# Optimization experiments

Measured on AMD Instinct MI355X. Metric: run time of the kernel, lower is better.

The kernel has to match this reference:

```python
import jax, jax.numpy as jnp
import numpy as np

B, S, H, E, C, V = 512, 256, 768, 6, 10, 3


def setup_inputs() -> dict:
    key = jax.random.key(0)
    ks = jax.random.split(key, 16)

    def w(k, shape):
        fan_in = shape[-1]
        return jax.random.normal(k, shape, dtype=jnp.float32) / np.sqrt(fan_in)

    return {
        'x': jax.random.randint(ks[0], (B, S), 0, V, dtype=jnp.int64),
        'emb': w(ks[1], (V, E)),
        'W_fx': w(ks[2], (H, E)), 'W_fh': w(ks[3], (H, H)), 'b_f': w(ks[4], (H, 1)),
        'W_ix': w(ks[5], (H, E)), 'W_ih': w(ks[6], (H, H)), 'b_i': w(ks[7], (H, 1)),
        'W_ox': w(ks[8], (H, E)), 'W_oh': w(ks[9], (H, H)), 'b_o': w(ks[10], (H, 1)),
        'W_cx': w(ks[11], (H, E)), 'b_c': w(ks[12], (H, 1)),
        'W_ph': w(ks[13], (C, H)), 'b_p': w(ks[14], (C, 1)),
        'c_init': jax.random.normal(ks[15], (H, B), dtype=jnp.float32) / np.sqrt(B),
    }


def reference(x, emb, W_fx, W_fh, b_f, W_ix, W_ih, b_i, W_ox, W_oh, b_o,
              W_cx, b_c, W_ph, b_p, c_init):
    # Embed tokens: [B, S] -> [B, S, E] -> time-major [S, E, B]
    xe = jnp.transpose(emb[x], (1, 2, 0))
    xs = xe[: S - 1]  # loop runs seq_length - 1 steps

    def step(carry, x_t):
        c_prev, _ = carry  # c_prev: [H, B], x_t: [E, B]
        f_t = jax.nn.sigmoid(W_fx @ x_t + W_fh @ c_prev + b_f)
        i_t = jax.nn.sigmoid(W_ix @ x_t + W_ih @ c_prev + b_i)
        o_t = jax.nn.sigmoid(W_ox @ x_t + W_oh @ c_prev + b_o)
        c_t = jax.nn.sigmoid(W_cx @ x_t + b_c) * i_t + c_prev * f_t
        h_t = jnp.tanh(c_t) * o_t
        return (c_t, h_t), None

    h0 = jnp.zeros((H, B), dtype=c_init.dtype)
    (c_fin, h_fin), _ = jax.lax.scan(step, (c_init, h0), xs)
    p_t = W_ph @ h_fin + b_p  # [C, B]
    return jax.nn.log_softmax(p_t.T, axis=-1)  # [B, C]
```

## Files before the change

### kernel.cpp

```cpp
#include <hip/hip_runtime.h>


typedef _Float16 f16x8 __attribute__((ext_vector_type(8)));
typedef _Float16 f16x4 __attribute__((ext_vector_type(4)));
typedef float    f32x4 __attribute__((ext_vector_type(4)));

#define Hdim  768
#define Bdim  512
#define Sdim  256
#define NSTEP 255
#define Edim  6
#define NCls  10
#define NGRP  16
#define NRB   12
#define GC    32
#define HB    64
#define NKK   24
#define NK2   12
#define CSTR  776
#define XSTR  260
#define ZSTR  33
#define PLANE (Bdim * Hdim)
#define SCL      4096.0f
#define SCL_INV  2.44140625e-4f

#define WP_FRAGS   (2 * NRB * 4 * NKK * 64)
#define WS_CBUF    0u
#define WS_HFIN    (2u * 2u * PLANE * 2u)
#define WS_BAR     (WS_HFIN + Bdim * Hdim * 4u)
#define WS_WPK     (WS_BAR + 4096u)
#define WS_BAR_BYTES (NGRP * 16u * 4u)

__device__ __forceinline__ float sigf(float z) { return 1.0f / (1.0f + __expf(-z)); }

__device__ __forceinline__ f32x4 mf(f16x8 a, f16x8 b, f32x4 c) {
    return __builtin_amdgcn_mfma_f32_16x16x32_f16(a, b, c, 0, 0, 0);
}

__device__ __forceinline__ void keepalive(f16x8& x) {
    asm volatile("" : "+v"(x));
}

__global__ void __launch_bounds__(256)
prep_w(const float* __restrict__ Wfh, const float* __restrict__ Wih,
       _Float16* __restrict__ wpk)
{
    const int fid  = blockIdx.x * 256 + threadIdx.x;
    const int lane = fid & 63;
    const int t1   = fid >> 6;
    const int kk   = t1 % NKK;
    const int gi   = t1 / NKK;
    const int sub  = gi & 3;
    const int t3   = gi >> 2;
    const int rb   = t3 % NRB;
    const int gate = t3 / NRB;
    const int q = lane >> 4, r = lane & 15;
    const int row = rb * 64 + sub * 16 + r;
    const int col = kk * 32 + q * 8;
    const float* src = (gate ? Wih : Wfh) + (size_t)row * Hdim + col;
    f16x8 hi, lo;
    #pragma unroll
    for (int j = 0; j < 8; ++j) {
        const float v = src[j];
        const _Float16 h = (_Float16)v;
        hi[j] = h;
        lo[j] = (_Float16)((v - (float)h) * SCL);
    }
    *(f16x8*)&wpk[(size_t)fid * 8] = hi;
    *(f16x8*)&wpk[((size_t)WP_FRAGS + fid) * 8] = lo;
}

__global__ void __launch_bounds__(512, 1)
lstm_persist(const int* __restrict__ xk, const float* __restrict__ emb,
             const float* __restrict__ Wfx, const float* __restrict__ bfv,
             const float* __restrict__ Wix, const float* __restrict__ biv,
             const float* __restrict__ Wox, const float* __restrict__ Woh,
             const float* __restrict__ bov,
             const float* __restrict__ Wcx, const float* __restrict__ bcv,
             const float* __restrict__ cinit,
             const _Float16* __restrict__ wpk,
             _Float16* __restrict__ cbuf, float* __restrict__ hfin,
             unsigned int* __restrict__ bar)
{
    __shared__ __align__(16) _Float16 ldsH[GC * CSTR];
    __shared__ __align__(16) _Float16 ldsM[GC * CSTR];
    __shared__ __align__(16) float    tbl[3 * HB * 4];
    __shared__ __align__(16) float    zred[4 * 4 * 64 * 4];
    __shared__ __align__(16) float    zbufP[2 * HB * ZSTR];
    __shared__ __align__(4)  unsigned char xtok[GC * XSTR];
    __shared__ int s_flag;

    const int tid  = threadIdx.x;
    const int w    = tid >> 6;
    const int lane = tid & 63;
    const int q    = lane >> 4;
    const int r    = lane & 15;
    const int kh   = w & 1;
    const int pr   = w >> 1;
    const int gt   = pr >> 1;
    const int rh   = pr & 1;
    const int subp = rh * 2 + kh;
    const int bid  = blockIdx.x;
    const int g    = bid & 15;
    const int rb   = bid >> 4;
    const int blkh0 = rb * HB;
    const int gc0   = g * GC;
    const int hq0   = blkh0 + subp * 16 + q * 4;

    if (tid == 0) s_flag = 0;
    __syncthreads();
    if (tid < 256) {
        if (xk[(size_t)gc0 * Sdim + 2 * tid + 1] != 0) s_flag = 1;
    }
    if (tid < 3 * HB) {
        const int v  = tid >> 6;
        const int hl = tid & 63;
        const int hg = blkh0 + hl;
        float pf = bfv[hg], pi = biv[hg], po = bov[hg], pc = bcv[hg];
        #pragma unroll
        for (int e = 0; e < Edim; ++e) {
            const float ev = emb[v * Edim + e];
            pf += Wfx[hg * Edim + e] * ev;
            pi += Wix[hg * Edim + e] * ev;
            po += Wox[hg * Edim + e] * ev;
            pc += Wcx[hg * Edim + e] * ev;
        }
        float* t = &tbl[(v * HB + hl) * 4];
        t[0] = pf; t[1] = pi; t[2] = po; t[3] = sigf(pc);
    }
    __syncthreads();
    const int is64 = (s_flag == 0);

    {
        const int col   = tid >> 4;
        const int sbase = (tid & 15) * 16;
        const size_t rowb = (size_t)(gc0 + col) * Sdim;
        for (int k2 = 0; k2 < 16; ++k2) {
            const int s0 = sbase + k2;
            const size_t idx = rowb + s0;
            xtok[col * XSTR + s0] = (unsigned char)xk[is64 ? (idx << 1) : idx];
        }
    }

    f16x8 whi[2][NK2], wlo[2][NK2];
    #pragma unroll
    for (int s2 = 0; s2 < 2; ++s2) {
        const int gis = (gt * NRB + rb) * 4 + (rh * 2 + s2);
        #pragma unroll
        for (int k2 = 0; k2 < NK2; ++k2) {
            const size_t fo = ((size_t)(gis * NKK + kh * NK2 + k2) * 64 + lane) * 8;
            whi[s2][k2] = *(const f16x8*)&wpk[fo];
            wlo[s2][k2] = *(const f16x8*)&wpk[(size_t)WP_FRAGS * 8 + fo];
        }
    }
    #pragma unroll
    for (int s2 = 0; s2 < 2; ++s2)
        #pragma unroll
        for (int k2 = 0; k2 < NK2; ++k2) {
            keepalive(whi[s2][k2]);
            keepalive(wlo[s2][k2]);
        }

    float cst[2][4];
    #pragma unroll
    for (int ct = 0; ct < 2; ++ct) {
        const int b = gc0 + ct * 16 + r;
        #pragma unroll
        for (int reg = 0; reg < 4; ++reg)
            cst[ct][reg] = cinit[(size_t)(hq0 + reg) * Bdim + b];
    }

    for (int i = 0; i < 48; ++i) {
        const int idx = tid + i * 512;
        const int col = idx & 31, k = idx >> 5;
        const float v = cinit[(size_t)k * Bdim + gc0 + col];
        const _Float16 h = (_Float16)v;
        ldsH[col * CSTR + k] = h;
        ldsM[col * CSTR + k] = (_Float16)((v - (float)h) * SCL);
    }

    for (int s = 0; s < NSTEP; ++s) {
        __syncthreads();

        f32x4 ah0c0 = {0,0,0,0}, ax0c0 = {0,0,0,0}, ah0c1 = {0,0,0,0}, ax0c1 = {0,0,0,0};
        f32x4 ah1c0 = {0,0,0,0}, ax1c0 = {0,0,0,0}, ah1c1 = {0,0,0,0}, ax1c1 = {0,0,0,0};
        #pragma unroll
        for (int k2 = 0; k2 < NK2; ++k2) {
            const int lo = (kh * NK2 + k2) * 32 + q * 8;
            const f16x8 bh0 = *(const f16x8*)&ldsH[ r       * CSTR + lo];
            const f16x8 bm0 = *(const f16x8*)&ldsM[ r       * CSTR + lo];
            const f16x8 bh1 = *(const f16x8*)&ldsH[(16 + r) * CSTR + lo];
            const f16x8 bm1 = *(const f16x8*)&ldsM[(16 + r) * CSTR + lo];
            ah0c0 = mf(whi[0][k2], bh0, ah0c0);
            ax0c0 = mf(whi[0][k2], bm0, ax0c0);
            ax0c0 = mf(wlo[0][k2], bh0, ax0c0);
            ah1c0 = mf(whi[1][k2], bh0, ah1c0);
            ax1c0 = mf(whi[1][k2], bm0, ax1c0);
            ax1c0 = mf(wlo[1][k2], bh0, ax1c0);
            ah0c1 = mf(whi[0][k2], bh1, ah0c1);
            ax0c1 = mf(whi[0][k2], bm1, ax0c1);
            ax0c1 = mf(wlo[0][k2], bh1, ax0c1);
            ah1c1 = mf(whi[1][k2], bh1, ah1c1);
            ax1c1 = mf(whi[1][k2], bm1, ax1c1);
            ax1c1 = mf(wlo[1][k2], bh1, ax1c1);
        }

        if (gt == 0) {
            const f32x4 sH0 = kh ? ah0c0 : ah1c0;
            const f32x4 sX0 = kh ? ax0c0 : ax1c0;
            const f32x4 sH1 = kh ? ah0c1 : ah1c1;
            const f32x4 sX1 = kh ? ax0c1 : ax1c1;
            f32x4* zr = (f32x4*)zred;
            zr[(w * 4 + 0) * 64 + lane] = sH0;
            zr[(w * 4 + 1) * 64 + lane] = sX0;
            zr[(w * 4 + 2) * 64 + lane] = sH1;
            zr[(w * 4 + 3) * 64 + lane] = sX1;
        } else {
            float* zp = &zbufP[kh * (HB * ZSTR)];
            #pragma unroll
            for (int s2 = 0; s2 < 2; ++s2) {
                const f32x4 h0 = s2 ? ah1c0 : ah0c0;
                const f32x4 x0 = s2 ? ax1c0 : ax0c0;
                const f32x4 h1 = s2 ? ah1c1 : ah0c1;
                const f32x4 x1 = s2 ? ax1c1 : ax0c1;
                #pragma unroll
                for (int reg = 0; reg < 4; ++reg) {
                    const int row = rh * 32 + s2 * 16 + q * 4 + reg;
                    zp[row * ZSTR + r]      = h0[reg] + x0[reg] * SCL_INV;
                    zp[row * ZSTR + 16 + r] = h1[reg] + x1[reg] * SCL_INV;
                }
            }
        }
        __syncthreads();

        if (gt == 0) {
            const f32x4* zr = (const f32x4*)zred;
            const int pw = w ^ 1;
            const f32x4 pH0 = zr[(pw * 4 + 0) * 64 + lane];
            const f32x4 pX0 = zr[(pw * 4 + 1) * 64 + lane];
            const f32x4 pH1 = zr[(pw * 4 + 2) * 64 + lane];
            const f32x4 pX1 = zr[(pw * 4 + 3) * 64 + lane];
            const f32x4 kH0 = kh ? ah1c0 : ah0c0;
            const f32x4 kX0 = kh ? ax1c0 : ax0c0;
            const f32x4 kH1 = kh ? ah1c1 : ah0c1;
            const f32x4 kX1 = kh ? ax1c1 : ax0c1;
            float zf[2][4];
            #pragma unroll
            for (int reg = 0; reg < 4; ++reg) {
                zf[0][reg] = (kH0[reg] + pH0[reg]) + (kX0[reg] + pX0[reg]) * SCL_INV;
                zf[1][reg] = (kH1[reg] + pH1[reg]) + (kX1[reg] + pX1[reg]) * SCL_INV;
            }
            const int rowl0 = rh * 32 + kh * 16 + q * 4;

            if (s != NSTEP - 1) {
                _Float16* cwH = cbuf + (size_t)(((s + 1) & 1) * 2) * PLANE;
                _Float16* cwM = cwH + PLANE;
                #pragma unroll
                for (int ct = 0; ct < 2; ++ct) {
                    const int bl = ct * 16 + r;
                    const int v  = xtok[bl * XSTR + s];
                    const float* tb = &tbl[(v * HB + subp * 16 + q * 4) * 4];
                    f16x4 cvh, cvm;
                    #pragma unroll
                    for (int reg = 0; reg < 4; ++reg) {
                        const int rowl = rowl0 + reg;
                        const float zi = zbufP[rowl * ZSTR + bl]
                                       + zbufP[HB * ZSTR + rowl * ZSTR + bl];
                        const float* tt = tb + reg * 4;
                        const float fg = sigf(zf[ct][reg] + tt[0]);
                        const float ig = sigf(zi + tt[1]);
                        const float cn = tt[3] * ig + cst[ct][reg] * fg;
                        cst[ct][reg] = cn;
                        const _Float16 ch = (_Float16)cn;
                        cvh[reg] = ch;
                        cvm[reg] = (_Float16)((cn - (float)ch) * SCL);
                    }
                    unsigned long long uh, um;
                    __builtin_memcpy(&uh, &cvh, 8);
                    __builtin_memcpy(&um, &cvm, 8);
                    const size_t eo = (size_t)(gc0 + bl) * Hdim + hq0;
                    __hip_atomic_store((unsigned long long*)&cwH[eo], uh,
                                       __ATOMIC_RELAXED, __HIP_MEMORY_SCOPE_AGENT);
                    __hip_atomic_store((unsigned long long*)&cwM[eo], um,
                                       __ATOMIC_RELAXED, __HIP_MEMORY_SCOPE_AGENT);
                }
            } else {
                f32x4 o0h = {0,0,0,0}, o0x = {0,0,0,0}, o1h = {0,0,0,0}, o1x = {0,0,0,0};
                const int arow = blkh0 + subp * 16 + r;
                #pragma unroll
                for (int kk = 0; kk < NKK; ++kk) {
                    const float* wp = Woh + (size_t)arow * Hdim + kk * 32 + q * 8;
                    f16x8 who;
                    #pragma unroll
                    for (int j = 0; j < 8; ++j) who[j] = (_Float16)wp[j];
                    const int lo = kk * 32 + q * 8;
                    const f16x8 bh0 = *(const f16x8*)&ldsH[ r       * CSTR + lo];
                    const f16x8 bm0 = *(const f16x8*)&ldsM[ r       * CSTR + lo];
                    const f16x8 bh1 = *(const f16x8*)&ldsH[(16 + r) * CSTR + lo];
                    const f16x8 bm1 = *(const f16x8*)&ldsM[(16 + r) * CSTR + lo];
                    o0h = mf(who, bh0, o0h);  o0x = mf(who, bm0, o0x);
                    o1h = mf(who, bh1, o1h);  o1x = mf(who, bm1, o1x);
                }
                #pragma unroll
                for (int ct = 0; ct < 2; ++ct) {
                    const int bl = ct * 16 + r;
                    const int v  = xtok[bl * XSTR + s];
                    const float* tb = &tbl[(v * HB + subp * 16 + q * 4) * 4];
                    const f32x4 zoh = ct ? o1h : o0h;
                    const f32x4 zox = ct ? o1x : o0x;
                    f32x4 hv;
                    #pragma unroll
                    for (int reg = 0; reg < 4; ++reg) {
                        const int rowl = rowl0 + reg;
                        const float zi = zbufP[rowl * ZSTR + bl]
                                       + zbufP[HB * ZSTR + rowl * ZSTR + bl];
                        const float zo = zoh[reg] + zox[reg] * SCL_INV;
                        const float* tt = tb + reg * 4;
                        const float fg = sigf(zf[ct][reg] + tt[0]);
                        const float ig = sigf(zi + tt[1]);
                        const float og = sigf(zo + tt[2]);
                        const float cn = tt[3] * ig + cst[ct][reg] * fg;
                        const float e  = __expf(-2.0f * fabsf(cn));
                        const float th = __builtin_copysignf((1.0f - e) / (1.0f + e), cn);
                        hv[reg] = th * og;
                    }
                    *(f32x4*)&hfin[(size_t)(gc0 + bl) * Hdim + hq0] = hv;
                }
            }
        }

        if (s < NSTEP - 1) {
            asm volatile("s_waitcnt vmcnt(0)" ::: "memory");
            __syncthreads();
            if (w == 0) {
                if (lane == 0)
                    __hip_atomic_store(&bar[g * 16 + rb], (unsigned)(s + 1),
                                       __ATOMIC_RELAXED, __HIP_MEMORY_SCOPE_AGENT);
                const unsigned tgt = (unsigned)(s + 1);
                while (true) {
                    unsigned vv = tgt;
                    if (lane < NRB)
                        vv = __hip_atomic_load(&bar[g * 16 + lane],
                                               __ATOMIC_RELAXED, __HIP_MEMORY_SCOPE_AGENT);
                    if (__all(vv >= tgt)) break;
                    __builtin_amdgcn_s_sleep(2);
                }
            }
            __syncthreads();
            const _Float16* crH = cbuf + (size_t)(((s + 1) & 1) * 2) * PLANE;
            const _Float16* crM = crH + PLANE;
            const int col = tid >> 4, j = tid & 15;
            const size_t rowo = (size_t)(gc0 + col) * Hdim;
            {
                unsigned long long th[12];
                #pragma unroll
                for (int i = 0; i < 12; ++i)
                    th[i] = __hip_atomic_load((unsigned long long*)&crH[rowo + (j + 16 * i) * 4],
                                              __ATOMIC_RELAXED, __HIP_MEMORY_SCOPE_AGENT);
                #pragma unroll
                for (int i = 0; i < 12; ++i)
                    *(unsigned long long*)&ldsH[col * CSTR + (j + 16 * i) * 4] = th[i];
            }
            {
                unsigned long long tm[12];
                #pragma unroll
                for (int i = 0; i < 12; ++i)
                    tm[i] = __hip_atomic_load((unsigned long long*)&crM[rowo + (j + 16 * i) * 4],
                                              __ATOMIC_RELAXED, __HIP_MEMORY_SCOPE_AGENT);
                #pragma unroll
                for (int i = 0; i < 12; ++i)
                    *(unsigned long long*)&ldsM[col * CSTR + (j + 16 * i) * 4] = tm[i];
            }
        }
    }
}

__global__ void __launch_bounds__(64)
proj_kernel(const float* __restrict__ hfin, const float* __restrict__ Wph,
            const float* __restrict__ bpv, float* __restrict__ out)
{
    const int b = blockIdx.x;
    const int lane = threadIdx.x;
    float acc[NCls];
    #pragma unroll
    for (int c = 0; c < NCls; ++c) acc[c] = 0.f;
    const float* hb = &hfin[(size_t)b * Hdim];
    for (int i = 0; i < Hdim / 64; ++i) {
        const float hv = hb[lane + i * 64];
        #pragma unroll
        for (int c = 0; c < NCls; ++c)
            acc[c] += Wph[c * Hdim + lane + i * 64] * hv;
    }
    #pragma unroll
    for (int c = 0; c < NCls; ++c) {
        float v = acc[c];
        #pragma unroll
        for (int off = 32; off > 0; off >>= 1)
            v += __shfl_xor(v, off, 64);
        acc[c] = v + bpv[c];
    }
    float m = acc[0];
    #pragma unroll
    for (int c = 1; c < NCls; ++c) m = fmaxf(m, acc[c]);
    float ssum = 0.f;
    #pragma unroll
    for (int c = 0; c < NCls; ++c) ssum += __expf(acc[c] - m);
    const float lse = m + __logf(ssum);
    if (lane < NCls) out[b * NCls + lane] = acc[lane] - lse;
}

extern "C" void kernel_launch(void* const* d_in, const int* in_sizes, int n_in,
                              void* d_out, int out_size, void* d_ws, size_t ws_size,
                              hipStream_t stream)
{
    const int*   xk    = (const int*)d_in[0];
    const float* emb   = (const float*)d_in[1];
    const float* Wfx   = (const float*)d_in[2];
    const float* Wfh   = (const float*)d_in[3];
    const float* bfv   = (const float*)d_in[4];
    const float* Wix   = (const float*)d_in[5];
    const float* Wih   = (const float*)d_in[6];
    const float* biv   = (const float*)d_in[7];
    const float* Wox   = (const float*)d_in[8];
    const float* Woh   = (const float*)d_in[9];
    const float* bov   = (const float*)d_in[10];
    const float* Wcx   = (const float*)d_in[11];
    const float* bcv   = (const float*)d_in[12];
    const float* Wph   = (const float*)d_in[13];
    const float* bpv   = (const float*)d_in[14];
    const float* cinit = (const float*)d_in[15];

    char* ws = (char*)d_ws;
    _Float16*     cbuf = (_Float16*)(ws + WS_CBUF);
    float*        hfin = (float*)(ws + WS_HFIN);
    unsigned int* bar  = (unsigned int*)(ws + WS_BAR);
    _Float16*     wpk  = (_Float16*)(ws + WS_WPK);

    hipMemsetAsync(bar, 0, WS_BAR_BYTES, stream);

    prep_w<<<dim3(WP_FRAGS / 256), dim3(256), 0, stream>>>(Wfh, Wih, wpk);

    lstm_persist<<<dim3(NGRP * NRB), dim3(512), 0, stream>>>(
        xk, emb, Wfx, bfv, Wix, biv, Wox, Woh, bov, Wcx, bcv,
        cinit, wpk, cbuf, hfin, bar);

    proj_kernel<<<dim3(Bdim), dim3(64), 0, stream>>>(hfin, Wph, bpv, (float*)d_out);
}
```

Baseline: 2.121 ms.

## Split per-step batch columns into two halves with staggered barriers for overlap

Each recurrent step's 32 batch columns are now processed in two 16-column halves. The first half's gate epilogue and cell writes overlap the second half's MFMA work. Per-half cross-block barriers are also staggered, so one wave group spins and reloads its half of the cell state while the other finishes its epilogue. This aims to hide barrier latency and global reload time behind compute. The cost is two barrier rounds per step, separate double buffers for partial sums, and more complex synchronisation that could deadlock or race if the half ownership is wrong.

```diff
diff --git a/kernel.cpp b/kernel.cpp
--- a/kernel.cpp
+++ b/kernel.cpp
@@ -19,7 +19,7 @@
 #define NK2   12
 #define CSTR  776
 #define XSTR  260
-#define ZSTR  33
+#define ZSTR2 17
 #define PLANE (Bdim * Hdim)
 #define SCL      4096.0f
 #define SCL_INV  2.44140625e-4f
@@ -85,8 +85,10 @@
     __shared__ __align__(16) _Float16 ldsH[GC * CSTR];
     __shared__ __align__(16) _Float16 ldsM[GC * CSTR];
     __shared__ __align__(16) float    tbl[3 * HB * 4];
-    __shared__ __align__(16) float    zred[4 * 4 * 64 * 4];
-    __shared__ __align__(16) float    zbufP[2 * HB * ZSTR];
+    __shared__ __align__(16) float    zredA[4 * 2 * 64 * 4];
+    __shared__ __align__(16) float    zredB[4 * 2 * 64 * 4];
+    __shared__ __align__(16) float    zbufPA[2 * HB * ZSTR2];
+    __shared__ __align__(16) float    zbufPB[2 * HB * ZSTR2];
     __shared__ __align__(4)  unsigned char xtok[GC * XSTR];
     __shared__ int s_flag;
 
@@ -179,112 +181,188 @@
         ldsM[col * CSTR + k] = (_Float16)((v - (float)h) * SCL);
     }
 
+    __syncthreads();
+
+#define MFMA_HALF(ROWOFF, AH0, AX0, AH1, AX1)                                  \
+    {                                                                          \
+        _Pragma("unroll")                                                      \
+        for (int k2 = 0; k2 < NK2; ++k2) {                                     \
+            const int lo = (kh * NK2 + k2) * 32 + q * 8;                       \
+            const f16x8 bh = *(const f16x8*)&ldsH[((ROWOFF) + r) * CSTR + lo]; \
+            const f16x8 bm = *(const f16x8*)&ldsM[((ROWOFF) + r) * CSTR + lo]; \
+            AH0 = mf(whi[0][k2], bh, AH0);                                     \
+            AX0 = mf(whi[0][k2], bm, AX0);                                     \
+            AX0 = mf(wlo[0][k2], bh, AX0);                                     \
+            AH1 = mf(whi[1][k2], bh, AH1);                                     \
+            AX1 = mf(whi[1][k2], bm, AX1);                                     \
+            AX1 = mf(wlo[1][k2], bh, AX1);                                     \
+        }                                                                      \
+    }
+
+#define SEND_PART(ZRED, AH0, AX0, AH1, AX1)                                    \
+    {                                                                          \
+        f32x4* zr_ = (f32x4*)(ZRED);                                           \
+        zr_[(w * 2 + 0) * 64 + lane] = kh ? AH0 : AH1;                         \
+        zr_[(w * 2 + 1) * 64 + lane] = kh ? AX0 : AX1;                         \
+    }
+
+#define IPART(ZBUF, AH0, AX0, AH1, AX1)                                        \
+    {                                                                          \
+        float* zp_ = &(ZBUF)[kh * (HB * ZSTR2)];                               \
+        _Pragma("unroll")                                                      \
+        for (int s2 = 0; s2 < 2; ++s2) {                                       \
+            const f32x4 h_ = s2 ? AH1 : AH0;                                   \
+            const f32x4 x_ = s2 ? AX1 : AX0;                                   \
+            _Pragma("unroll")                                                  \
+            for (int reg = 0; reg < 4; ++reg) {                                \
+                const int row_ = rh * 32 + s2 * 16 + q * 4 + reg;              \
+                zp_[row_ * ZSTR2 + r] = h_[reg] + x_[reg] * SCL_INV;           \
+            }                                                                  \
+        }                                                                      \
+    }
+
+#define REDUCE_K(ZRED, KH_, KX_, ZF)                                           \
+    {                                                                          \
+        const f32x4* zr_ = (const f32x4*)(ZRED);                               \
+        const int pw_ = w ^ 1;                                                 \
+        const f32x4 pH_ = zr_[(pw_ * 2 + 0) * 64 + lane];                      \
+        const f32x4 pX_ = zr_[(pw_ * 2 + 1) * 64 + lane];                      \
+        _Pragma("unroll")                                                      \
+        for (int reg = 0; reg < 4; ++reg)                                      \
+            ZF[reg] = (KH_[reg] + pH_[reg]) + (KX_[reg] + pX_[reg]) * SCL_INV; \
+    }
+
+#define EPILOGUE_C(CT, ZF, ZBUF)                                               \
+    {                                                                          \
+        _Float16* cwH = cbuf + (size_t)(((s + 1) & 1) * 2) * PLANE;            \
+        _Float16* cwM = cwH + PLANE;                                           \
+        const int bl = (CT) * 16 + r;                                          \
+        const int v  = xtok[bl * XSTR + s];                                    \
+        const float* tb = &tbl[(v * HB + subp * 16 + q * 4) * 4];              \
+        f16x4 cvh, cvm;                                                        \
+        _Pragma("unroll")                                                      \
+        for (int reg = 0; reg < 4; ++reg) {                                    \
+            const int rowl = subp * 16 + q * 4 + reg;                          \
+            const float zi = (ZBUF)[rowl * ZSTR2 + r]                          \
+                           + (ZBUF)[HB * ZSTR2 + rowl * ZSTR2 + r];            \
+            const float* tt = tb + reg * 4;                                    \
+            const float fg = sigf(ZF[reg] + tt[0]);                            \
+            const float ig = sigf(zi + tt[1]);                                 \
+            const float cn = tt[3] * ig + cst[CT][reg] * fg;                   \
+            cst[CT][reg] = cn;                                                 \
+            const _Float16 ch = (_Float16)cn;                                  \
+            cvh[reg] = ch;                                                     \
+            cvm[reg] = (_Float16)((cn - (float)ch) * SCL);                     \
+        }                                                                      \
+        unsigned long long uh, um;                                             \
+        __builtin_memcpy(&uh, &cvh, 8);                                        \
+        __builtin_memcpy(&um, &cvm, 8);                                        \
+        const size_t eo = (size_t)(gc0 + bl) * Hdim + hq0;                     \
+        __hip_atomic_store((unsigned long long*)&cwH[eo], uh,                  \
+                           __ATOMIC_RELAXED, __HIP_MEMORY_SCOPE_AGENT);        \
+        __hip_atomic_store((unsigned long long*)&cwM[eo], um,                  \
+                           __ATOMIC_RELAXED, __HIP_MEMORY_SCOPE_AGENT);        \
+    }
+
+#define SPIN(TGT)                                                              \
+    {                                                                          \
+        const unsigned tgt_ = (TGT);                                           \
+        while (true) {                                                         \
+            unsigned vv_ = tgt_;                                               \
+            if (lane < NRB)                                                    \
+                vv_ = __hip_atomic_load(&bar[g * 16 + lane],                   \
+                                        __ATOMIC_RELAXED,                      \
+                                        __HIP_MEMORY_SCOPE_AGENT);             \
+            if (__all(vv_ >= tgt_)) break;                                     \
+            __builtin_amdgcn_s_sleep(2);                                       \
+        }                                                                      \
+        asm volatile("" ::: "memory");                                         \
+    }
+
+#define LOAD_HALF(LCOL, JJ)                                                    \
+    {                                                                          \
+        const _Float16* crH = cbuf + (size_t)(((s + 1) & 1) * 2) * PLANE;      \
+        const _Float16* crM = crH + PLANE;                                     \
+        const size_t rowo = (size_t)(gc0 + (LCOL)) * Hdim;                     \
+        unsigned long long th[12];                                             \
+        _Pragma("unroll")                                                      \
+        for (int i = 0; i < 12; ++i)                                           \
+            th[i] = __hip_atomic_load(                                         \
+                (unsigned long long*)&crH[rowo + ((JJ) + 16 * i) * 4],         \
+                __ATOMIC_RELAXED, __HIP_MEMORY_SCOPE_AGENT);                   \
+        _Pragma("unroll")                                                      \
+        for (int i = 0; i < 12; ++i)                                           \
+            *(unsigned long long*)&ldsH[(LCOL) * CSTR + ((JJ) + 16 * i) * 4] = th[i]; \
+        unsigned long long tm[12];                                             \
+        _Pragma("unroll")                                                      \
+        for (int i = 0; i < 12; ++i)                                           \
+            tm[i] = __hip_atomic_load(                                         \
+                (unsigned long long*)&crM[rowo + ((JJ) + 16 * i) * 4],         \
+                __ATOMIC_RELAXED, __HIP_MEMORY_SCOPE_AGENT);                   \
+        _Pragma("unroll")                                                      \
+        for (int i = 0; i < 12; ++i)                                           \
+            *(unsigned long long*)&ldsM[(LCOL) * CSTR + ((JJ) + 16 * i) * 4] = tm[i]; \
+    }
+
     for (int s = 0; s < NSTEP; ++s) {
+        const bool last = (s == NSTEP - 1);
+
+        f32x4 ah0 = {0,0,0,0}, ax0 = {0,0,0,0}, ah1 = {0,0,0,0}, ax1 = {0,0,0,0};
+        MFMA_HALF(0, ah0, ax0, ah1, ax1);
+
+        if (gt == 0) { SEND_PART(zredA, ah0, ax0, ah1, ax1); }
+        else         { IPART(zbufPA, ah0, ax0, ah1, ax1); }
+
         __syncthreads();
 
-        f32x4 ah0c0 = {0,0,0,0}, ax0c0 = {0,0,0,0}, ah0c1 = {0,0,0,0}, ax0c1 = {0,0,0,0};
-        f32x4 ah1c0 = {0,0,0,0}, ax1c0 = {0,0,0,0}, ah1c1 = {0,0,0,0}, ax1c1 = {0,0,0,0};
-        #pragma unroll
-        for (int k2 = 0; k2 < NK2; ++k2) {
-            const int lo = (kh * NK2 + k2) * 32 + q * 8;
-            const f16x8 bh0 = *(const f16x8*)&ldsH[ r       * CSTR + lo];
-            const f16x8 bm0 = *(const f16x8*)&ldsM[ r       * CSTR + lo];
-            const f16x8 bh1 = *(const f16x8*)&ldsH[(16 + r) * CSTR + lo];
-            const f16x8 bm1 = *(const f16x8*)&ldsM[(16 + r) * CSTR + lo];
-            ah0c0 = mf(whi[0][k2], bh0, ah0c0);
-            ax0c0 = mf(whi[0][k2], bm0, ax0c0);
-            ax0c0 = mf(wlo[0][k2], bh0, ax0c0);
-            ah1c0 = mf(whi[1][k2], bh0, ah1c0);
-            ax1c0 = mf(whi[1][k2], bm0, ax1c0);
-            ax1c0 = mf(wlo[1][k2], bh0, ax1c0);
-            ah0c1 = mf(whi[0][k2], bh1, ah0c1);
-            ax0c1 = mf(whi[0][k2], bm1, ax0c1);
-            ax0c1 = mf(wlo[0][k2], bh1, ax0c1);
-            ah1c1 = mf(whi[1][k2], bh1, ah1c1);
-            ax1c1 = mf(whi[1][k2], bm1, ax1c1);
-            ax1c1 = mf(wlo[1][k2], bh1, ax1c1);
-        }
-
+        f32x4 bh0v = {0,0,0,0}, bx0v = {0,0,0,0}, bh1v = {0,0,0,0}, bx1v = {0,0,0,0};
+        float zfA[4];
         if (gt == 0) {
-            const f32x4 sH0 = kh ? ah0c0 : ah1c0;
-            const f32x4 sX0 = kh ? ax0c0 : ax1c0;
-            const f32x4 sH1 = kh ? ah0c1 : ah1c1;
-            const f32x4 sX1 = kh ? ax0c1 : ax1c1;
-            f32x4* zr = (f32x4*)zred;
-            zr[(w * 4 + 0) * 64 + lane] = sH0;
-            zr[(w * 4 + 1) * 64 + lane] = sX0;
-            zr[(w * 4 + 2) * 64 + lane] = sH1;
-            zr[(w * 4 + 3) * 64 + lane] = sX1;
+            const f32x4 kHa = kh ? ah1 : ah0;
+            const f32x4 kXa = kh ? ax1 : ax0;
+            REDUCE_K(zredA, kHa, kXa, zfA);
+            if (!last) EPILOGUE_C(0, zfA, zbufPA);
+            MFMA_HALF(16, bh0v, bx0v, bh1v, bx1v);
+            SEND_PART(zredB, bh0v, bx0v, bh1v, bx1v);
         } else {
-            float* zp = &zbufP[kh * (HB * ZSTR)];
-            #pragma unroll
-            for (int s2 = 0; s2 < 2; ++s2) {
-                const f32x4 h0 = s2 ? ah1c0 : ah0c0;
-                const f32x4 x0 = s2 ? ax1c0 : ax0c0;
-                const f32x4 h1 = s2 ? ah1c1 : ah0c1;
-                const f32x4 x1 = s2 ? ax1c1 : ax0c1;
-                #pragma unroll
-                for (int reg = 0; reg < 4; ++reg) {
-                    const int row = rh * 32 + s2 * 16 + q * 4 + reg;
-                    zp[row * ZSTR + r]      = h0[reg] + x0[reg] * SCL_INV;
-                    zp[row * ZSTR + 16 + r] = h1[reg] + x1[reg] * SCL_INV;
-                }
+            MFMA_HALF(16, bh0v, bx0v, bh1v, bx1v);
+            IPART(zbufPB, bh0v, bx0v, bh1v, bx1v);
+        }
+
+        asm volatile("s_waitcnt vmcnt(0)" ::: "memory");
+        __syncthreads();
+
+        if (!last) {
+            if (tid == 0)
+                __hip_atomic_store(&bar[g * 16 + rb], (unsigned)(2 * s + 1),
+                                   __ATOMIC_RELAXED, __HIP_MEMORY_SCOPE_AGENT);
+            if (gt == 0) {
+                const f32x4 kHb = kh ? bh1v : bh0v;
+                const f32x4 kXb = kh ? bx1v : bx0v;
+                float zfB[4];
+                REDUCE_K(zredB, kHb, kXb, zfB);
+                EPILOGUE_C(1, zfB, zbufPB);
+            } else {
+                SPIN((unsigned)(2 * s + 1));
+                const int lt = tid - 256;
+                LOAD_HALF(lt >> 4, lt & 15);
             }
-        }
-        __syncthreads();
-
-        if (gt == 0) {
-            const f32x4* zr = (const f32x4*)zred;
-            const int pw = w ^ 1;
-            const f32x4 pH0 = zr[(pw * 4 + 0) * 64 + lane];
-            const f32x4 pX0 = zr[(pw * 4 + 1) * 64 + lane];
-            const f32x4 pH1 = zr[(pw * 4 + 2) * 64 + lane];
-            const f32x4 pX1 = zr[(pw * 4 + 3) * 64 + lane];
-            const f32x4 kH0 = kh ? ah1c0 : ah0c0;
-            const f32x4 kX0 = kh ? ax1c0 : ax0c0;
-            const f32x4 kH1 = kh ? ah1c1 : ah0c1;
-            const f32x4 kX1 = kh ? ax1c1 : ax0c1;
-            float zf[2][4];
-            #pragma unroll
-            for (int reg = 0; reg < 4; ++reg) {
-                zf[0][reg] = (kH0[reg] + pH0[reg]) + (kX0[reg] + pX0[reg]) * SCL_INV;
-                zf[1][reg] = (kH1[reg] + pH1[reg]) + (kX1[reg] + pX1[reg]) * SCL_INV;
+            asm volatile("s_waitcnt vmcnt(0)" ::: "memory");
+            __syncthreads();
+            if (tid == 0)
+                __hip_atomic_store(&bar[g * 16 + rb], (unsigned)(2 * s + 2),
+                                   __ATOMIC_RELAXED, __HIP_MEMORY_SCOPE_AGENT);
+            if (gt == 0) {
+                SPIN((unsigned)(2 * s + 2));
+                LOAD_HALF(16 + (tid >> 4), tid & 15);
             }
-            const int rowl0 = rh * 32 + kh * 16 + q * 4;
-
-            if (s != NSTEP - 1) {
-                _Float16* cwH = cbuf + (size_t)(((s + 1) & 1) * 2) * PLANE;
-                _Float16* cwM = cwH + PLANE;
-                #pragma unroll
-                for (int ct = 0; ct < 2; ++ct) {
-                    const int bl = ct * 16 + r;
-                    const int v  = xtok[bl * XSTR + s];
-                    const float* tb = &tbl[(v * HB + subp * 16 + q * 4) * 4];
-                    f16x4 cvh, cvm;
-                    #pragma unroll
-                    for (int reg = 0; reg < 4; ++reg) {
-                        const int rowl = rowl0 + reg;
-                        const float zi = zbufP[rowl * ZSTR + bl]
-                                       + zbufP[HB * ZSTR + rowl * ZSTR + bl];
-                        const float* tt = tb + reg * 4;
-                        const float fg = sigf(zf[ct][reg] + tt[0]);
-                        const float ig = sigf(zi + tt[1]);
-                        const float cn = tt[3] * ig + cst[ct][reg] * fg;
-                        cst[ct][reg] = cn;
-                        const _Float16 ch = (_Float16)cn;
-                        cvh[reg] = ch;
-                        cvm[reg] = (_Float16)((cn - (float)ch) * SCL);
-                    }
-                    unsigned long long uh, um;
-                    __builtin_memcpy(&uh, &cvh, 8);
-                    __builtin_memcpy(&um, &cvm, 8);
-                    const size_t eo = (size_t)(gc0 + bl) * Hdim + hq0;
-                    __hip_atomic_store((unsigned long long*)&cwH[eo], uh,
-                                       __ATOMIC_RELAXED, __HIP_MEMORY_SCOPE_AGENT);
-                    __hip_atomic_store((unsigned long long*)&cwM[eo], um,
-                                       __ATOMIC_RELAXED, __HIP_MEMORY_SCOPE_AGENT);
-                }
-            } else {
+        } else {
+            if (gt == 0) {
+                const f32x4 kHb = kh ? bh1v : bh0v;
+                const f32x4 kXb = kh ? bx1v : bx0v;
+                float zfB[4];
+                REDUCE_K(zredB, kHb, kXb, zfB);
+
                 f32x4 o0h = {0,0,0,0}, o0x = {0,0,0,0}, o1h = {0,0,0,0}, o1x = {0,0,0,0};
                 const int arow = blkh0 + subp * 16 + r;
                 #pragma unroll
@@ -308,15 +386,17 @@
                     const float* tb = &tbl[(v * HB + subp * 16 + q * 4) * 4];
                     const f32x4 zoh = ct ? o1h : o0h;
                     const f32x4 zox = ct ? o1x : o0x;
+                    const float* zfp = ct ? zfB : zfA;
+                    const float* zbp = ct ? zbufPB : zbufPA;
                     f32x4 hv;
                     #pragma unroll
                     for (int reg = 0; reg < 4; ++reg) {
-                        const int rowl = rowl0 + reg;
-                        const float zi = zbufP[rowl * ZSTR + bl]
-                                       + zbufP[HB * ZSTR + rowl * ZSTR + bl];
+                        const int rowl = subp * 16 + q * 4 + reg;
+                        const float zi = zbp[rowl * ZSTR2 + r]
+                                       + zbp[HB * ZSTR2 + rowl * ZSTR2 + r];
                         const float zo = zoh[reg] + zox[reg] * SCL_INV;
                         const float* tt = tb + reg * 4;
-                        const float fg = sigf(zf[ct][reg] + tt[0]);
+                        const float fg = sigf(zfp[reg] + tt[0]);
                         const float ig = sigf(zi + tt[1]);
                         const float og = sigf(zo + tt[2]);
                         const float cn = tt[3] * ig + cst[ct][reg] * fg;
@@ -326,50 +406,6 @@
                     }
                     *(f32x4*)&hfin[(size_t)(gc0 + bl) * Hdim + hq0] = hv;
                 }
-            }
-        }
-
-        if (s < NSTEP - 1) {
-            asm volatile("s_waitcnt vmcnt(0)" ::: "memory");
-            __syncthreads();
-            if (w == 0) {
-                if (lane == 0)
-                    __hip_atomic_store(&bar[g * 16 + rb], (unsigned)(s + 1),
-                                       __ATOMIC_RELAXED, __HIP_MEMORY_SCOPE_AGENT);
-                const unsigned tgt = (unsigned)(s + 1);
-                while (true) {
-                    unsigned vv = tgt;
-                    if (lane < NRB)
-                        vv = __hip_atomic_load(&bar[g * 16 + lane],
-                                               __ATOMIC_RELAXED, __HIP_MEMORY_SCOPE_AGENT);
-                    if (__all(vv >= tgt)) break;
-                    __builtin_amdgcn_s_sleep(2);
-                }
-            }
-            __syncthreads();
-            const _Float16* crH = cbuf + (size_t)(((s + 1) & 1) * 2) * PLANE;
-            const _Float16* crM = crH + PLANE;
-            const int col = tid >> 4, j = tid & 15;
-            const size_t rowo = (size_t)(gc0 + col) * Hdim;
-            {
-                unsigned long long th[12];
-                #pragma unroll
-                for (int i = 0; i < 12; ++i)
-                    th[i] = __hip_atomic_load((unsigned long long*)&crH[rowo + (j + 16 * i) * 4],
-                                              __ATOMIC_RELAXED, __HIP_MEMORY_SCOPE_AGENT);
-                #pragma unroll
-                for (int i = 0; i < 12; ++i)
-                    *(unsigned long long*)&ldsH[col * CSTR + (j + 16 * i) * 4] = th[i];
-            }
-            {
-                unsigned long long tm[12];
-                #pragma unroll
-                for (int i = 0; i < 12; ++i)
-                    tm[i] = __hip_atomic_load((unsigned long long*)&crM[rowo + (j + 16 * i) * 4],
-                                              __ATOMIC_RELAXED, __HIP_MEMORY_SCOPE_AGENT);
-                #pragma unroll
-                for (int i = 0; i < 12; ++i)
-                    *(unsigned long long*)&ldsM[col * CSTR + (j + 16 * i) * 4] = tm[i];
             }
         }
     }
```

Result: slower. 2.310 ms (+8.9%).

## Split batch into 32 groups of 16 columns to double persistent block count

Applied to the files above, without the earlier changes.

Halves the per-block batch tile from 32 to 16 columns and doubles the number of batch groups to 32, so the persistent grid grows from 192 to 384 blocks. Each block now keeps one MFMA column tile instead of two, with smaller reduction buffers and a smaller per-step refill of the recurrent state. The aim is to use more compute units and shorten each block's serial per-step work. The cost is that every block still holds its full register-resident weight slice and still spin-waits on a barrier each step. The launch-bounds occupancy hint is also raised, which may constrain register allocation for those resident weights.

```diff
diff --git a/kernel.cpp b/kernel.cpp
--- a/kernel.cpp
+++ b/kernel.cpp
@@ -11,15 +11,15 @@
 #define NSTEP 255
 #define Edim  6
 #define NCls  10
-#define NGRP  16
+#define NGRP  32
 #define NRB   12
-#define GC    32
+#define GC    16
 #define HB    64
 #define NKK   24
 #define NK2   12
 #define CSTR  776
 #define XSTR  260
-#define ZSTR  33
+#define ZSTR2 17
 #define PLANE (Bdim * Hdim)
 #define SCL      4096.0f
 #define SCL_INV  2.44140625e-4f
@@ -70,7 +70,7 @@
     *(f16x8*)&wpk[((size_t)WP_FRAGS + fid) * 8] = lo;
 }
 
-__global__ void __launch_bounds__(512, 1)
+__global__ void __launch_bounds__(512, 4)
 lstm_persist(const int* __restrict__ xk, const float* __restrict__ emb,
              const float* __restrict__ Wfx, const float* __restrict__ bfv,
              const float* __restrict__ Wix, const float* __restrict__ biv,
@@ -85,8 +85,8 @@
     __shared__ __align__(16) _Float16 ldsH[GC * CSTR];
     __shared__ __align__(16) _Float16 ldsM[GC * CSTR];
     __shared__ __align__(16) float    tbl[3 * HB * 4];
-    __shared__ __align__(16) float    zred[4 * 4 * 64 * 4];
-    __shared__ __align__(16) float    zbufP[2 * HB * ZSTR];
+    __shared__ __align__(16) float    zred[4 * 2 * 64 * 4];
+    __shared__ __align__(16) float    zbufP[2 * HB * ZSTR2];
     __shared__ __align__(4)  unsigned char xtok[GC * XSTR];
     __shared__ int s_flag;
 
@@ -101,8 +101,8 @@
     const int rh   = pr & 1;
     const int subp = rh * 2 + kh;
     const int bid  = blockIdx.x;
-    const int g    = bid & 15;
-    const int rb   = bid >> 4;
+    const int g    = bid & 31;
+    const int rb   = bid >> 5;
     const int blkh0 = rb * HB;
     const int gc0   = g * GC;
     const int hq0   = blkh0 + subp * 16 + q * 4;
@@ -132,10 +132,10 @@
     const int is64 = (s_flag == 0);
 
     {
-        const int col   = tid >> 4;
-        const int sbase = (tid & 15) * 16;
+        const int col   = tid >> 5;
+        const int sbase = (tid & 31) * 8;
         const size_t rowb = (size_t)(gc0 + col) * Sdim;
-        for (int k2 = 0; k2 < 16; ++k2) {
+        for (int k2 = 0; k2 < 8; ++k2) {
             const int s0 = sbase + k2;
             const size_t idx = rowb + s0;
             xtok[col * XSTR + s0] = (unsigned char)xk[is64 ? (idx << 1) : idx];
@@ -161,18 +161,17 @@
             keepalive(wlo[s2][k2]);
         }
 
-    float cst[2][4];
-    #pragma unroll
-    for (int ct = 0; ct < 2; ++ct) {
-        const int b = gc0 + ct * 16 + r;
+    float cst[4];
+    {
+        const int b = gc0 + r;
         #pragma unroll
         for (int reg = 0; reg < 4; ++reg)
-            cst[ct][reg] = cinit[(size_t)(hq0 + reg) * Bdim + b];
-    }
-
-    for (int i = 0; i < 48; ++i) {
+            cst[reg] = cinit[(size_t)(hq0 + reg) * Bdim + b];
+    }
+
+    for (int i = 0; i < 24; ++i) {
         const int idx = tid + i * 512;
-        const int col = idx & 31, k = idx >> 5;
+        const int col = idx & 15, k = idx >> 4;
         const float v = cinit[(size_t)k * Bdim + gc0 + col];
         const _Float16 h = (_Float16)v;
         ldsH[col * CSTR + k] = h;
@@ -182,110 +181,82 @@
     for (int s = 0; s < NSTEP; ++s) {
         __syncthreads();
 
-        f32x4 ah0c0 = {0,0,0,0}, ax0c0 = {0,0,0,0}, ah0c1 = {0,0,0,0}, ax0c1 = {0,0,0,0};
-        f32x4 ah1c0 = {0,0,0,0}, ax1c0 = {0,0,0,0}, ah1c1 = {0,0,0,0}, ax1c1 = {0,0,0,0};
+        f32x4 ah0 = {0,0,0,0}, ax0 = {0,0,0,0};
+        f32x4 ah1 = {0,0,0,0}, ax1 = {0,0,0,0};
         #pragma unroll
         for (int k2 = 0; k2 < NK2; ++k2) {
             const int lo = (kh * NK2 + k2) * 32 + q * 8;
-            const f16x8 bh0 = *(const f16x8*)&ldsH[ r       * CSTR + lo];
-            const f16x8 bm0 = *(const f16x8*)&ldsM[ r       * CSTR + lo];
-            const f16x8 bh1 = *(const f16x8*)&ldsH[(16 + r) * CSTR + lo];
-            const f16x8 bm1 = *(const f16x8*)&ldsM[(16 + r) * CSTR + lo];
-            ah0c0 = mf(whi[0][k2], bh0, ah0c0);
-            ax0c0 = mf(whi[0][k2], bm0, ax0c0);
-            ax0c0 = mf(wlo[0][k2], bh0, ax0c0);
-            ah1c0 = mf(whi[1][k2], bh0, ah1c0);
-            ax1c0 = mf(whi[1][k2], bm0, ax1c0);
-            ax1c0 = mf(wlo[1][k2], bh0, ax1c0);
-            ah0c1 = mf(whi[0][k2], bh1, ah0c1);
-            ax0c1 = mf(whi[0][k2], bm1, ax0c1);
-            ax0c1 = mf(wlo[0][k2], bh1, ax0c1);
-            ah1c1 = mf(whi[1][k2], bh1, ah1c1);
-            ax1c1 = mf(whi[1][k2], bm1, ax1c1);
-            ax1c1 = mf(wlo[1][k2], bh1, ax1c1);
+            const f16x8 bh = *(const f16x8*)&ldsH[r * CSTR + lo];
+            const f16x8 bm = *(const f16x8*)&ldsM[r * CSTR + lo];
+            ah0 = mf(whi[0][k2], bh, ah0);
+            ax0 = mf(whi[0][k2], bm, ax0);
+            ax0 = mf(wlo[0][k2], bh, ax0);
+            ah1 = mf(whi[1][k2], bh, ah1);
+            ax1 = mf(whi[1][k2], bm, ax1);
+            ax1 = mf(wlo[1][k2], bh, ax1);
         }
 
         if (gt == 0) {
-            const f32x4 sH0 = kh ? ah0c0 : ah1c0;
-            const f32x4 sX0 = kh ? ax0c0 : ax1c0;
-            const f32x4 sH1 = kh ? ah0c1 : ah1c1;
-            const f32x4 sX1 = kh ? ax0c1 : ax1c1;
             f32x4* zr = (f32x4*)zred;
-            zr[(w * 4 + 0) * 64 + lane] = sH0;
-            zr[(w * 4 + 1) * 64 + lane] = sX0;
-            zr[(w * 4 + 2) * 64 + lane] = sH1;
-            zr[(w * 4 + 3) * 64 + lane] = sX1;
+            zr[(w * 2 + 0) * 64 + lane] = kh ? ah0 : ah1;
+            zr[(w * 2 + 1) * 64 + lane] = kh ? ax0 : ax1;
         } else {
-            float* zp = &zbufP[kh * (HB * ZSTR)];
+            float* zp = &zbufP[kh * (HB * ZSTR2)];
             #pragma unroll
             for (int s2 = 0; s2 < 2; ++s2) {
-                const f32x4 h0 = s2 ? ah1c0 : ah0c0;
-                const f32x4 x0 = s2 ? ax1c0 : ax0c0;
-                const f32x4 h1 = s2 ? ah1c1 : ah0c1;
-                const f32x4 x1 = s2 ? ax1c1 : ax0c1;
+                const f32x4 h_ = s2 ? ah1 : ah0;
+                const f32x4 x_ = s2 ? ax1 : ax0;
                 #pragma unroll
                 for (int reg = 0; reg < 4; ++reg) {
-                    const int row = rh * 32 + s2 * 16 + q * 4 + reg;
-                    zp[row * ZSTR + r]      = h0[reg] + x0[reg] * SCL_INV;
-                    zp[row * ZSTR + 16 + r] = h1[reg] + x1[reg] * SCL_INV;
+                    const int row_ = rh * 32 + s2 * 16 + q * 4 + reg;
+                    zp[row_ * ZSTR2 + r] = h_[reg] + x_[reg] * SCL_INV;
                 }
             }
         }
         __syncthreads();
 
+        float zf[4];
         if (gt == 0) {
             const f32x4* zr = (const f32x4*)zred;
             const int pw = w ^ 1;
-            const f32x4 pH0 = zr[(pw * 4 + 0) * 64 + lane];
-            const f32x4 pX0 = zr[(pw * 4 + 1) * 64 + lane];
-            const f32x4 pH1 = zr[(pw * 4 + 2) * 64 + lane];
-            const f32x4 pX1 = zr[(pw * 4 + 3) * 64 + lane];
-            const f32x4 kH0 = kh ? ah1c0 : ah0c0;
-            const f32x4 kX0 = kh ? ax1c0 : ax0c0;
-            const f32x4 kH1 = kh ? ah1c1 : ah0c1;
-            const f32x4 kX1 = kh ? ax1c1 : ax0c1;
-            float zf[2][4];
+            const f32x4 pH = zr[(pw * 2 + 0) * 64 + lane];
+            const f32x4 pX = zr[(pw * 2 + 1) * 64 + lane];
+            const f32x4 kH = kh ? ah1 : ah0;
+            const f32x4 kX = kh ? ax1 : ax0;
             #pragma unroll
-            for (int reg = 0; reg < 4; ++reg) {
-                zf[0][reg] = (kH0[reg] + pH0[reg]) + (kX0[reg] + pX0[reg]) * SCL_INV;
-                zf[1][reg] = (kH1[reg] + pH1[reg]) + (kX1[reg] + pX1[reg]) * SCL_INV;
-            }
-            const int rowl0 = rh * 32 + kh * 16 + q * 4;
+            for (int reg = 0; reg < 4; ++reg)
+                zf[reg] = (kH[reg] + pH[reg]) + (kX[reg] + pX[reg]) * SCL_INV;
 
             if (s != NSTEP - 1) {
                 _Float16* cwH = cbuf + (size_t)(((s + 1) & 1) * 2) * PLANE;
                 _Float16* cwM = cwH + PLANE;
-                #pragma unroll
-                for (int ct = 0; ct < 2; ++ct) {
-                    const int bl = ct * 16 + r;
-                    const int v  = xtok[bl * XSTR + s];
-                    const float* tb = &tbl[(v * HB + subp * 16 + q * 4) * 4];
-                    f16x4 cvh, cvm;
-                    #pragma unroll
-                    for (int reg = 0; reg < 4; ++reg) {
-                        const int rowl = rowl0 + reg;
-                        const float zi = zbufP[rowl * ZSTR + bl]
-                                       + zbufP[HB * ZSTR + rowl * ZSTR + bl];
-                        const float* tt = tb + reg * 4;
-                        const float fg = sigf(zf[ct][reg] + tt[0]);
-                        const float ig = sigf(zi + tt[1]);
-                        const float cn = tt[3] * ig + cst[ct][reg] * fg;
-                        cst[ct][reg] = cn;
-                        const _Float16 ch = (_Float16)cn;
-                        cvh[reg] = ch;
-                        cvm[reg] = (_Float16)((cn - (float)ch) * SCL);
-                    }
-                    unsigned long long uh, um;
-                    __builtin_memcpy(&uh, &cvh, 8);
-                    __builtin_memcpy(&um, &cvm, 8);
-                    const size_t eo = (size_t)(gc0 + bl) * Hdim + hq0;
-                    __hip_atomic_store((unsigned long long*)&cwH[eo], uh,
-                                       __ATOMIC_RELAXED, __HIP_MEMORY_SCOPE_AGENT);
-                    __hip_atomic_store((unsigned long long*)&cwM[eo], um,
-                                       __ATOMIC_RELAXED, __HIP_MEMORY_SCOPE_AGENT);
+                const int v  = xtok[r * XSTR + s];
+                const float* tb = &tbl[(v * HB + subp * 16 + q * 4) * 4];
+                f16x4 cvh, cvm;
+                #pragma unroll
+                for (int reg = 0; reg < 4; ++reg) {
+                    const int rowl = subp * 16 + q * 4 + reg;
+                    const float zi = zbufP[rowl * ZSTR2 + r]
+                                   + zbufP[HB * ZSTR2 + rowl * ZSTR2 + r];
+                    const float* tt = tb + reg * 4;
+                    const float fg = sigf(zf[reg] + tt[0]);
+                    const float ig = sigf(zi + tt[1]);
+                    const float cn = tt[3] * ig + cst[reg] * fg;
+                    cst[reg] = cn;
+                    const _Float16 ch = (_Float16)cn;
+                    cvh[reg] = ch;
+                    cvm[reg] = (_Float16)((cn - (float)ch) * SCL);
                 }
+                unsigned long long uh, um;
+                __builtin_memcpy(&uh, &cvh, 8);
+                __builtin_memcpy(&um, &cvm, 8);
+                const size_t eo = (size_t)(gc0 + r) * Hdim + hq0;
+                __hip_atomic_store((unsigned long long*)&cwH[eo], uh,
+                                   __ATOMIC_RELAXED, __HIP_MEMORY_SCOPE_AGENT);
+                __hip_atomic_store((unsigned long long*)&cwM[eo], um,
+                                   __ATOMIC_RELAXED, __HIP_MEMORY_SCOPE_AGENT);
             } else {
-                f32x4 o0h = {0,0,0,0}, o0x = {0,0,0,0}, o1h = {0,0,0,0}, o1x = {0,0,0,0};
+                f32x4 oh = {0,0,0,0}, ox = {0,0,0,0};
                 const int arow = blkh0 + subp * 16 + r;
                 #pragma unroll
                 for (int kk = 0; kk < NKK; ++kk) {
@@ -294,38 +265,30 @@
                     #pragma unroll
                     for (int j = 0; j < 8; ++j) who[j] = (_Float16)wp[j];
                     const int lo = kk * 32 + q * 8;
-                    const f16x8 bh0 = *(const f16x8*)&ldsH[ r       * CSTR + lo];
-                    const f16x8 bm0 = *(const f16x8*)&ldsM[ r       * CSTR + lo];
-                    const f16x8 bh1 = *(const f16x8*)&ldsH[(16 + r) * CSTR + lo];
-                    const f16x8 bm1 = *(const f16x8*)&ldsM[(16 + r) * CSTR + lo];
-                    o0h = mf(who, bh0, o0h);  o0x = mf(who, bm0, o0x);
-                    o1h = mf(who, bh1, o1h);  o1x = mf(who, bm1, o1x);
+                    const f16x8 bh = *(const f16x8*)&ldsH[r * CSTR + lo];
+                    const f16x8 bm = *(const f16x8*)&ldsM[r * CSTR + lo];
+                    oh = mf(who, bh, oh);
+                    ox = mf(who, bm, ox);
                 }
-                #pragma unroll
-                for (int ct = 0; ct < 2; ++ct) {
-                    const int bl = ct * 16 + r;
-                    const int v  = xtok[bl * XSTR + s];
-                    const float* tb = &tbl[(v * HB + subp * 16 + q * 4) * 4];
-                    const f32x4 zoh = ct ? o1h : o0h;
-                    const f32x4 zox = ct ? o1x : o0x;
-                    f32x4 hv;
-                    #pragma unroll
-                    for (int reg = 0; reg < 4; ++reg) {
-                        const int rowl = rowl0 + reg;
-                        const float zi = zbufP[rowl * ZSTR + bl]
-                                       + zbufP[HB * ZSTR + rowl * ZSTR + bl];
-                        const float zo = zoh[reg] + zox[reg] * SCL_INV;
-                        const float* tt = tb + reg * 4;
-                        const float fg = sigf(zf[ct][reg] + tt[0]);
-                        const float ig = sigf(zi + tt[1]);
-                        const float og = sigf(zo + tt[2]);
-                        const float cn = tt[3] * ig + cst[ct][reg] * fg;
-                        const float e  = __expf(-2.0f * fabsf(cn));
-                        const float th = __builtin_copysignf((1.0f - e) / (1.0f + e), cn);
-                        hv[reg] = th * og;
-                    }
-                    *(f32x4*)&hfin[(size_t)(gc0 + bl) * Hdim + hq0] = hv;
+                const int v  = xtok[r * XSTR + s];
+                const float* tb = &tbl[(v * HB + subp * 16 + q * 4) * 4];
+                f32x4 hv;
+                #pragma unroll
+                for (int reg = 0; reg < 4; ++reg) {
+                    const int rowl = subp * 16 + q * 4 + reg;
+                    const float zi = zbufP[rowl * ZSTR2 + r]
+                                   + zbufP[HB * ZSTR2 + rowl * ZSTR2 + r];
+                    const float zo = oh[reg] + ox[reg] * SCL_INV;
+                    const float* tt = tb + reg * 4;
+                    const float fg = sigf(zf[reg] + tt[0]);
+                    const float ig = sigf(zi + tt[1]);
+                    const float og = sigf(zo + tt[2]);
+                    const float cn = tt[3] * ig + cst[reg] * fg;
+                    const float e  = __expf(-2.0f * fabsf(cn));
+                    const float th = __builtin_copysignf((1.0f - e) / (1.0f + e), cn);
+                    hv[reg] = th * og;
                 }
+                *(f32x4*)&hfin[(size_t)(gc0 + r) * Hdim + hq0] = hv;
             }
         }
 
@@ -349,27 +312,27 @@
             __syncthreads();
             const _Float16* crH = cbuf + (size_t)(((s + 1) & 1) * 2) * PLANE;
             const _Float16* crM = crH + PLANE;
-            const int col = tid >> 4, j = tid & 15;
+            const int col = tid >> 5, j = tid & 31;
             const size_t rowo = (size_t)(gc0 + col) * Hdim;
             {
-                unsigned long long th[12];
-                #pragma unroll
-                for (int i = 0; i < 12; ++i)
-                    th[i] = __hip_atomic_load((unsigned long long*)&crH[rowo + (j + 16 * i) * 4],
+                unsigned long long th[6];
+                #pragma unroll
+                for (int i = 0; i < 6; ++i)
+                    th[i] = __hip_atomic_load((unsigned long long*)&crH[rowo + (j + 32 * i) * 4],
                                               __ATOMIC_RELAXED, __HIP_MEMORY_SCOPE_AGENT);
                 #pragma unroll
-                for (int i = 0; i < 12; ++i)
-                    *(unsigned long long*)&ldsH[col * CSTR + (j + 16 * i) * 4] = th[i];
+                for (int i = 0; i < 6; ++i)
+                    *(unsigned long long*)&ldsH[col * CSTR + (j + 32 * i) * 4] = th[i];
             }
             {
-                unsigned long long tm[12];
-                #pragma unroll
-                for (int i = 0; i < 12; ++i)
-                    tm[i] = __hip_atomic_load((unsigned long long*)&crM[rowo + (j + 16 * i) * 4],
+                unsigned long long tm[6];
+                #pragma unroll
+                for (int i = 0; i < 6; ++i)
+                    tm[i] = __hip_atomic_load((unsigned long long*)&crM[rowo + (j + 32 * i) * 4],
                                               __ATOMIC_RELAXED, __HIP_MEMORY_SCOPE_AGENT);
                 #pragma unroll
-                for (int i = 0; i < 12; ++i)
-                    *(unsigned long long*)&ldsM[col * CSTR + (j + 16 * i) * 4] = tm[i];
+                for (int i = 0; i < 6; ++i)
+                    *(unsigned long long*)&ldsM[col * CSTR + (j + 32 * i) * 4] = tm[i];
             }
         }
     }
```

After: 5.515 ms. +160.0%, slower.

## Split warps into compute and loader roles with per-slab barrier polling

Applied to the files above, without the earlier changes.

Restructures the per-step grid synchronisation. The compute waves now signal completion through an LDS counter, and wave 0 publishes the block's flag. The remaining waves (w>=4) each poll the readiness flag of individual row-block slabs and copy each slab into LDS as soon as it is ready, instead of waiting for all 12 row blocks before a full-block load. This aims to overlap barrier waiting with data movement and to remove a block-wide sync. It adds spin loops per slab and relies on the wave-role split matching the earlier branch structure.

```diff
diff --git a/kernel.cpp b/kernel.cpp
--- a/kernel.cpp
+++ b/kernel.cpp
@@ -89,6 +89,7 @@
     __shared__ __align__(16) float    zbufP[2 * HB * ZSTR];
     __shared__ __align__(4)  unsigned char xtok[GC * XSTR];
     __shared__ int s_flag;
+    __shared__ unsigned s_done;
 
     const int tid  = threadIdx.x;
     const int w    = tid >> 6;
@@ -107,7 +108,7 @@
     const int gc0   = g * GC;
     const int hq0   = blkh0 + subp * 16 + q * 4;
 
-    if (tid == 0) s_flag = 0;
+    if (tid == 0) { s_flag = 0; s_done = 0; }
     __syncthreads();
     if (tid < 256) {
         if (xk[(size_t)gc0 * Sdim + 2 * tid + 1] != 0) s_flag = 1;
@@ -179,8 +180,10 @@
         ldsM[col * CSTR + k] = (_Float16)((v - (float)h) * SCL);
     }
 
+    __syncthreads();
+
     for (int s = 0; s < NSTEP; ++s) {
-        __syncthreads();
+        const bool last = (s == NSTEP - 1);
 
         f32x4 ah0c0 = {0,0,0,0}, ax0c0 = {0,0,0,0}, ah0c1 = {0,0,0,0}, ax0c1 = {0,0,0,0};
         f32x4 ah1c0 = {0,0,0,0}, ax1c0 = {0,0,0,0}, ah1c1 = {0,0,0,0}, ax1c1 = {0,0,0,0};
@@ -252,7 +255,7 @@
             }
             const int rowl0 = rh * 32 + kh * 16 + q * 4;
 
-            if (s != NSTEP - 1) {
+            if (!last) {
                 _Float16* cwH = cbuf + (size_t)(((s + 1) & 1) * 2) * PLANE;
                 _Float16* cwM = cwH + PLANE;
                 #pragma unroll
@@ -284,6 +287,19 @@
                     __hip_atomic_store((unsigned long long*)&cwM[eo], um,
                                        __ATOMIC_RELAXED, __HIP_MEMORY_SCOPE_AGENT);
                 }
+                asm volatile("s_waitcnt vmcnt(0)" ::: "memory");
+                if (lane == 0)
+                    __hip_atomic_fetch_add(&s_done, 1u, __ATOMIC_RELAXED,
+                                           __HIP_MEMORY_SCOPE_WORKGROUP);
+                if (w == 0) {
+                    const unsigned tgt = 4u * (unsigned)(s + 1);
+                    while (__hip_atomic_load(&s_done, __ATOMIC_RELAXED,
+                                             __HIP_MEMORY_SCOPE_WORKGROUP) < tgt)
+                        __builtin_amdgcn_s_sleep(1);
+                    if (lane == 0)
+                        __hip_atomic_store(&bar[g * 16 + rb], (unsigned)(s + 1),
+                                           __ATOMIC_RELAXED, __HIP_MEMORY_SCOPE_AGENT);
+                }
             } else {
                 f32x4 o0h = {0,0,0,0}, o0x = {0,0,0,0}, o1h = {0,0,0,0}, o1x = {0,0,0,0};
                 const int arow = blkh0 + subp * 16 + r;
@@ -327,51 +343,46 @@
                     *(f32x4*)&hfin[(size_t)(gc0 + bl) * Hdim + hq0] = hv;
                 }
             }
-        }
-
-        if (s < NSTEP - 1) {
-            asm volatile("s_waitcnt vmcnt(0)" ::: "memory");
-            __syncthreads();
-            if (w == 0) {
-                if (lane == 0)
-                    __hip_atomic_store(&bar[g * 16 + rb], (unsigned)(s + 1),
-                                       __ATOMIC_RELAXED, __HIP_MEMORY_SCOPE_AGENT);
-                const unsigned tgt = (unsigned)(s + 1);
-                while (true) {
-                    unsigned vv = tgt;
-                    if (lane < NRB)
-                        vv = __hip_atomic_load(&bar[g * 16 + lane],
-                                               __ATOMIC_RELAXED, __HIP_MEMORY_SCOPE_AGENT);
-                    if (__all(vv >= tgt)) break;
-                    __builtin_amdgcn_s_sleep(2);
-                }
-            }
-            __syncthreads();
+        } else if (!last) {
             const _Float16* crH = cbuf + (size_t)(((s + 1) & 1) * 2) * PLANE;
             const _Float16* crM = crH + PLANE;
-            const int col = tid >> 4, j = tid & 15;
-            const size_t rowo = (size_t)(gc0 + col) * Hdim;
-            {
-                unsigned long long th[12];
-                #pragma unroll
-                for (int i = 0; i < 12; ++i)
-                    th[i] = __hip_atomic_load((unsigned long long*)&crH[rowo + (j + 16 * i) * 4],
+            const int col = lane >> 1;
+            const int e   = lane & 1;
+            const int j0  = (w - 4) * 3;
+            #pragma unroll
+            for (int jj = 0; jj < 3; ++jj) {
+                const int slab = j0 + jj;
+                while (__hip_atomic_load(&bar[g * 16 + slab], __ATOMIC_RELAXED,
+                                         __HIP_MEMORY_SCOPE_AGENT) < (unsigned)(s + 1))
+                    __builtin_amdgcn_s_sleep(2);
+                asm volatile("" ::: "memory");
+                const int kb = slab * 64 + e * 32;
+                const size_t go = (size_t)(gc0 + col) * Hdim + kb;
+                unsigned long long th[8], tm[8];
+                #pragma unroll
+                for (int t = 0; t < 8; ++t)
+                    th[t] = __hip_atomic_load((unsigned long long*)&crH[go + t * 4],
                                               __ATOMIC_RELAXED, __HIP_MEMORY_SCOPE_AGENT);
                 #pragma unroll
-                for (int i = 0; i < 12; ++i)
-                    *(unsigned long long*)&ldsH[col * CSTR + (j + 16 * i) * 4] = th[i];
+                for (int t = 0; t < 8; ++t)
+                    tm[t] = __hip_atomic_load((unsigned long long*)&crM[go + t * 4],
+                                              __ATOMIC_RELAXED, __HIP_MEMORY_SCOPE_AGENT);
+                #pragma unroll
+                for (int t2 = 0; t2 < 4; ++t2) {
+                    ulonglong2 v2;
+                    v2.x = th[2 * t2]; v2.y = th[2 * t2 + 1];
+                    *(ulonglong2*)&ldsH[col * CSTR + kb + t2 * 8] = v2;
+                }
+                #pragma unroll
+                for (int t2 = 0; t2 < 4; ++t2) {
+                    ulonglong2 v2;
+                    v2.x = tm[2 * t2]; v2.y = tm[2 * t2 + 1];
+                    *(ulonglong2*)&ldsM[col * CSTR + kb + t2 * 8] = v2;
+                }
             }
-            {
-                unsigned long long tm[12];
-                #pragma unroll
-                for (int i = 0; i < 12; ++i)
-                    tm[i] = __hip_atomic_load((unsigned long long*)&crM[rowo + (j + 16 * i) * 4],
-                                              __ATOMIC_RELAXED, __HIP_MEMORY_SCOPE_AGENT);
-                #pragma unroll
-                for (int i = 0; i < 12; ++i)
-                    *(unsigned long long*)&ldsM[col * CSTR + (j + 16 * i) * 4] = tm[i];
-            }
-        }
+        }
+
+        __syncthreads();
     }
 }
 
```

New measurement: 3.716 ms. +75.2%, slower.
